# Kernel tuning notes

Measured on AMD Instinct MI355X. Metric: run time of the kernel, lower is better.

The kernel has to match this reference:

```python
import jax, jax.numpy as jnp
import numpy as np

EPS = 1e-7  # keras backend epsilon


def setup_inputs() -> dict:
    key = jax.random.key(0)
    k1, k2, k3, k4, k5 = jax.random.split(key, 5)
    B, L, D, U = 8, 1024, 256, 256
    seq_data = jax.random.normal(k1, (B, L, D), dtype=jnp.float32)
    graph = jax.random.uniform(k2, (B, L, L), dtype=jnp.float32)
    scale = 1.0 / np.sqrt(D)
    e_weight = jax.random.normal(k3, (D, U), dtype=jnp.float32) * scale
    Wx = jax.random.normal(k4, (U, U), dtype=jnp.float32) * scale
    Wh = jax.random.normal(k5, (U, U), dtype=jnp.float32) * scale
    b = jnp.zeros((U,), dtype=jnp.float32)
    return {"seq_data": seq_data, "graph": graph, "e_weight": e_weight,
            "Wx": Wx, "Wh": Wh, "b": b}


def reference(seq_data, graph, e_weight, Wx, Wh, b):
    # beta = seq_data @ e_weight : (B, L, U)
    beta = jnp.einsum('bld,du->blu', seq_data, e_weight)
    # normalize_graph_output: divide by out-degree sum over axis 2 -> (B, L)
    norm = jnp.maximum(jnp.sum(graph, axis=2), EPS)
    beta = beta / norm[:, :, None]
    # K.batch_dot(beta(B,L,U), graph(B,L,M), axes=(1,1)) -> (B,U,M), then
    # permute (0,2,1) -> (B,M,U); fused as a single einsum.
    agg = jnp.einsum('blu,blm->bmu', beta, graph)  # (B, L, U)
    B, L, U = agg.shape
    h0 = jnp.zeros((B, U), dtype=agg.dtype)  # get_initial_state: zeros

    def step(h, x):  # SimpleRNNCell: h' = tanh(x Wx + h Wh + b)
        h = jnp.tanh(x @ Wx + h @ Wh + b)
        return h, h

    _, ys = jax.lax.scan(step, h0, jnp.swapaxes(agg, 0, 1))  # (L, B, U)
    return jnp.swapaxes(ys, 0, 1)  # (B, L, U)
```

## Files before the change

### kernel.cpp

```cpp
#include <hip/hip_runtime.h>
#include <hip/hip_bf16.h>


typedef unsigned short u16;
typedef unsigned int u32;
typedef __bf16 bf16_t;
typedef __bf16 bf16x8 __attribute__((ext_vector_type(8)));
typedef float f32x4 __attribute__((ext_vector_type(4)));
typedef unsigned short u16x8 __attribute__((ext_vector_type(8)));
typedef unsigned short u16x4 __attribute__((ext_vector_type(4)));

#define LDS_P 72
#define HP_B  288

struct HiLo { u16 hi, lo; };

__device__ __forceinline__ u16 f2bf(float f) {
  bf16_t h = (bf16_t)f;
  return __builtin_bit_cast(u16, h);
}
__device__ __forceinline__ HiLo splitf(float v) {
  bf16_t h = (bf16_t)v;
  HiLo r;
  r.hi = __builtin_bit_cast(u16, h);
  r.lo = f2bf(v - (float)h);
  return r;
}
__device__ __forceinline__ float tanh_fast(float x) {
  float ax = fabsf(x);
  float e  = __expf(-2.0f * ax);
  float t  = __fdividef(1.0f - e, 1.0f + e);
  return copysignf(t, x);
}
__device__ __forceinline__ void sync_lds_only() {
  __asm__ volatile("s_waitcnt lgkmcnt(0)\ns_barrier" ::: "memory");
}

__global__ void transpose_split3(const float* __restrict__ s0, u16* __restrict__ h0, u16* __restrict__ l0,
                                 const float* __restrict__ s1, u16* __restrict__ h1, u16* __restrict__ l1,
                                 const float* __restrict__ s2, u16* __restrict__ h2o, u16* __restrict__ l2o) {
  const int u = blockIdx.x, d = threadIdx.x;
  const float* s; u16 *dh, *dl;
  if (blockIdx.y == 0)      { s = s0; dh = h0;  dl = l0; }
  else if (blockIdx.y == 1) { s = s1; dh = h1;  dl = l1; }
  else                      { s = s2; dh = h2o; dl = l2o; }
  HiLo r = splitf(s[d * 256 + u]);
  dh[u * 256 + d] = r.hi;
  dl[u * 256 + d] = r.lo;
}

__global__ void rowsum_norm(const float* __restrict__ graph, float* __restrict__ rnorm) {
  const int wave = threadIdx.x >> 6, lane = threadIdx.x & 63;
  const int row = blockIdx.x * 4 + wave;
  const float* p = graph + (size_t)row * 1024 + lane * 16;
  float s = 0.f;
#pragma unroll
  for (int c = 0; c < 4; c++) {
    f32x4 v = *(const f32x4*)(p + c * 4);
#pragma unroll
    for (int j = 0; j < 4; j++) s += v[j];
  }
#pragma unroll
  for (int off = 32; off > 0; off >>= 1) s += __shfl_xor(s, off);
  if (lane == 0) rnorm[row] = 1.0f / fmaxf(s, 1e-7f);
}

__global__ __launch_bounds__(256, 2) void gemm_beta(const float* __restrict__ seq,
                                                    const u16* __restrict__ Eth,
                                                    const u16* __restrict__ Etl,
                                                    const float* __restrict__ rnorm,
                                                    u16* __restrict__ betaTh,
                                                    u16* __restrict__ betaTl) {
  __shared__ u16 Ah[64 * LDS_P], Al[64 * LDS_P];
  __shared__ u16 Bh[64 * LDS_P], Bl[64 * LDS_P];
  const int t = threadIdx.x;
  const int wave = t >> 6, lane = t & 63, quad = lane >> 4, l16 = lane & 15;
  const int r0 = blockIdx.x * 64, n0 = blockIdx.y * 64;
  f32x4 acc[4];
#pragma unroll
  for (int i = 0; i < 4; i++) acc[i] = (f32x4){0.f, 0.f, 0.f, 0.f};

  for (int kb = 0; kb < 256; kb += 64) {
#pragma unroll
    for (int cc = 0; cc < 4; cc++) {
      int c = t + cc * 256;
      int r = c >> 4, c4 = c & 15;
      f32x4 v = *(const f32x4*)(seq + (size_t)(r0 + r) * 256 + kb + c4 * 4);
      u16x4 hi, lo;
#pragma unroll
      for (int j = 0; j < 4; j++) {
        HiLo s = splitf(v[j]);
        hi[j] = s.hi; lo[j] = s.lo;
      }
      *(u16x4*)(Ah + r * LDS_P + c4 * 4) = hi;
      *(u16x4*)(Al + r * LDS_P + c4 * 4) = lo;
    }
#pragma unroll
    for (int cc = 0; cc < 2; cc++) {
      int c = t + cc * 256;
      int r = c >> 3, c8 = c & 7;
      *(u16x8*)(Bh + r * LDS_P + c8 * 8) =
          *(const u16x8*)(Eth + (size_t)(n0 + r) * 256 + kb + c8 * 8);
      *(u16x8*)(Bl + r * LDS_P + c8 * 8) =
          *(const u16x8*)(Etl + (size_t)(n0 + r) * 256 + kb + c8 * 8);
    }
    __syncthreads();
#pragma unroll
    for (int kk = 0; kk < 64; kk += 32) {
      bf16x8 ah = __builtin_bit_cast(bf16x8, *(const u16x8*)(Ah + (wave * 16 + l16) * LDS_P + kk + quad * 8));
      bf16x8 al = __builtin_bit_cast(bf16x8, *(const u16x8*)(Al + (wave * 16 + l16) * LDS_P + kk + quad * 8));
#pragma unroll
      for (int tN = 0; tN < 4; tN++) {
        bf16x8 bh = __builtin_bit_cast(bf16x8, *(const u16x8*)(Bh + (tN * 16 + l16) * LDS_P + kk + quad * 8));
        bf16x8 bl = __builtin_bit_cast(bf16x8, *(const u16x8*)(Bl + (tN * 16 + l16) * LDS_P + kk + quad * 8));
        acc[tN] = __builtin_amdgcn_mfma_f32_16x16x32_bf16(ah, bh, acc[tN], 0, 0, 0);
        acc[tN] = __builtin_amdgcn_mfma_f32_16x16x32_bf16(ah, bl, acc[tN], 0, 0, 0);
        acc[tN] = __builtin_amdgcn_mfma_f32_16x16x32_bf16(al, bh, acc[tN], 0, 0, 0);
      }
    }
    __syncthreads();
  }
  const int rbase = r0 + wave * 16 + quad * 4;
  float rn[4];
#pragma unroll
  for (int i = 0; i < 4; i++) rn[i] = rnorm[rbase + i];
  const int bI = rbase >> 10, lI = rbase & 1023;
#pragma unroll
  for (int tN = 0; tN < 4; tN++) {
    int u = n0 + tN * 16 + l16;
    u16x4 hv, lv;
#pragma unroll
    for (int i = 0; i < 4; i++) {
      HiLo s = splitf(acc[tN][i] * rn[i]);
      hv[i] = s.hi; lv[i] = s.lo;
    }
    size_t off = ((size_t)bI << 18) + (size_t)u * 1024 + lI;
    *(u16x4*)(betaTh + off) = hv;
    *(u16x4*)(betaTl + off) = lv;
  }
}

__global__ __launch_bounds__(256, 2) void gemm_agg(const float* __restrict__ graph,
                                                   const u16* __restrict__ betaTh,
                                                   const u16* __restrict__ betaTl,
                                                   float* __restrict__ agg) {
  __shared__ u16 Ah[64 * LDS_P], Al[64 * LDS_P];
  __shared__ u16 Bh[64 * LDS_P], Bl[64 * LDS_P];
  const int t = threadIdx.x;
  const int wave = t >> 6, lane = t & 63, quad = lane >> 4, l16 = lane & 15;
  const int m0 = blockIdx.x * 64, n0 = blockIdx.y * 64, b = blockIdx.z;
  const float* g = graph + (size_t)b * (1024 * 1024);
  const size_t bt = (size_t)b << 18;
  f32x4 acc[4];
#pragma unroll
  for (int i = 0; i < 4; i++) acc[i] = (f32x4){0.f, 0.f, 0.f, 0.f};

  for (int kb = 0; kb < 1024; kb += 64) {
#pragma unroll
    for (int cc = 0; cc < 4; cc++) {
      int c = t + cc * 256;
      int r = c >> 4, c4 = c & 15;
      f32x4 v = *(const f32x4*)(g + (size_t)(kb + r) * 1024 + m0 + c4 * 4);
#pragma unroll
      for (int j = 0; j < 4; j++) {
        HiLo s = splitf(v[j]);
        Ah[(c4 * 4 + j) * LDS_P + r] = s.hi;
        Al[(c4 * 4 + j) * LDS_P + r] = s.lo;
      }
    }
#pragma unroll
    for (int cc = 0; cc < 2; cc++) {
      int c = t + cc * 256;
      int r = c >> 3, c8 = c & 7;
      *(u16x8*)(Bh + r * LDS_P + c8 * 8) =
          *(const u16x8*)(betaTh + bt + (size_t)(n0 + r) * 1024 + kb + c8 * 8);
      *(u16x8*)(Bl + r * LDS_P + c8 * 8) =
          *(const u16x8*)(betaTl + bt + (size_t)(n0 + r) * 1024 + kb + c8 * 8);
    }
    __syncthreads();
#pragma unroll
    for (int kk = 0; kk < 64; kk += 32) {
      bf16x8 ah = __builtin_bit_cast(bf16x8, *(const u16x8*)(Ah + (wave * 16 + l16) * LDS_P + kk + quad * 8));
      bf16x8 al = __builtin_bit_cast(bf16x8, *(const u16x8*)(Al + (wave * 16 + l16) * LDS_P + kk + quad * 8));
#pragma unroll
      for (int tN = 0; tN < 4; tN++) {
        bf16x8 bh = __builtin_bit_cast(bf16x8, *(const u16x8*)(Bh + (tN * 16 + l16) * LDS_P + kk + quad * 8));
        bf16x8 bl = __builtin_bit_cast(bf16x8, *(const u16x8*)(Bl + (tN * 16 + l16) * LDS_P + kk + quad * 8));
        acc[tN] = __builtin_amdgcn_mfma_f32_16x16x32_bf16(ah, bh, acc[tN], 0, 0, 0);
        acc[tN] = __builtin_amdgcn_mfma_f32_16x16x32_bf16(ah, bl, acc[tN], 0, 0, 0);
        acc[tN] = __builtin_amdgcn_mfma_f32_16x16x32_bf16(al, bh, acc[tN], 0, 0, 0);
      }
    }
    __syncthreads();
  }
  const int mbase = m0 + wave * 16 + quad * 4;
#pragma unroll
  for (int tN = 0; tN < 4; tN++) {
    int u = n0 + tN * 16 + l16;
#pragma unroll
    for (int i = 0; i < 4; i++)
      agg[((size_t)b * 1024 + mbase + i) * 256 + u] = acc[tN][i];
  }
}

__global__ __launch_bounds__(256, 2) void gemm_xpre(const float* __restrict__ agg,
                                                    const u16* __restrict__ Wxth,
                                                    const u16* __restrict__ Wxtl,
                                                    const float* __restrict__ bias,
                                                    float* __restrict__ Xpre) {
  __shared__ u16 Ah[64 * LDS_P], Al[64 * LDS_P];
  __shared__ u16 Bh[64 * LDS_P], Bl[64 * LDS_P];
  const int t = threadIdx.x;
  const int wave = t >> 6, lane = t & 63, quad = lane >> 4, l16 = lane & 15;
  const int r0 = blockIdx.x * 64, n0 = blockIdx.y * 64;
  f32x4 acc[4];
#pragma unroll
  for (int i = 0; i < 4; i++) acc[i] = (f32x4){0.f, 0.f, 0.f, 0.f};

  for (int kb = 0; kb < 256; kb += 64) {
#pragma unroll
    for (int cc = 0; cc < 4; cc++) {
      int c = t + cc * 256;
      int r = c >> 4, c4 = c & 15;
      f32x4 v = *(const f32x4*)(agg + (size_t)(r0 + r) * 256 + kb + c4 * 4);
      u16x4 hi, lo;
#pragma unroll
      for (int j = 0; j < 4; j++) {
        HiLo s = splitf(v[j]);
        hi[j] = s.hi; lo[j] = s.lo;
      }
      *(u16x4*)(Ah + r * LDS_P + c4 * 4) = hi;
      *(u16x4*)(Al + r * LDS_P + c4 * 4) = lo;
    }
#pragma unroll
    for (int cc = 0; cc < 2; cc++) {
      int c = t + cc * 256;
      int r = c >> 3, c8 = c & 7;
      *(u16x8*)(Bh + r * LDS_P + c8 * 8) =
          *(const u16x8*)(Wxth + (size_t)(n0 + r) * 256 + kb + c8 * 8);
      *(u16x8*)(Bl + r * LDS_P + c8 * 8) =
          *(const u16x8*)(Wxtl + (size_t)(n0 + r) * 256 + kb + c8 * 8);
    }
    __syncthreads();
#pragma unroll
    for (int kk = 0; kk < 64; kk += 32) {
      bf16x8 ah = __builtin_bit_cast(bf16x8, *(const u16x8*)(Ah + (wave * 16 + l16) * LDS_P + kk + quad * 8));
      bf16x8 al = __builtin_bit_cast(bf16x8, *(const u16x8*)(Al + (wave * 16 + l16) * LDS_P + kk + quad * 8));
#pragma unroll
      for (int tN = 0; tN < 4; tN++) {
        bf16x8 bh = __builtin_bit_cast(bf16x8, *(const u16x8*)(Bh + (tN * 16 + l16) * LDS_P + kk + quad * 8));
        bf16x8 bl = __builtin_bit_cast(bf16x8, *(const u16x8*)(Bl + (tN * 16 + l16) * LDS_P + kk + quad * 8));
        acc[tN] = __builtin_amdgcn_mfma_f32_16x16x32_bf16(ah, bh, acc[tN], 0, 0, 0);
        acc[tN] = __builtin_amdgcn_mfma_f32_16x16x32_bf16(ah, bl, acc[tN], 0, 0, 0);
        acc[tN] = __builtin_amdgcn_mfma_f32_16x16x32_bf16(al, bh, acc[tN], 0, 0, 0);
      }
    }
    __syncthreads();
  }
  const int rbase = r0 + wave * 16 + quad * 4;
  const int bI = rbase >> 10;
#pragma unroll
  for (int tN = 0; tN < 4; tN++) {
    int u = n0 + tN * 16 + l16;
    float bu = bias[u];
#pragma unroll
    for (int i = 0; i < 4; i++) {
      int mI = (rbase + i) & 1023;
      Xpre[((size_t)mI * 8 + bI) * 256 + u] = acc[tN][i] + bu;
    }
  }
}

__global__ __launch_bounds__(512, 2) void rnn_scan(const u16* __restrict__ Whth,
                                                   const u16* __restrict__ Whtl,
                                                   const float* __restrict__ Xpre,
                                                   float* __restrict__ out) {
  __shared__ u16 h2[2][2 * HP_B];
  const int b = blockIdx.x;
  const int t = threadIdx.x;
  const int w = t >> 6, lane = t & 63, quad = lane >> 4, l16 = lane & 15;
  const int colbase = w * 32;
  int col[2];
  col[0] = colbase + l16;
  col[1] = colbase + 16 + l16;
  const bool epi = (quad == 0);

  bf16x8 bwh[2][8], bwl[2][8];
#pragma unroll
  for (int tN = 0; tN < 2; tN++) {
    const u16* wph = Whth + (size_t)(colbase + tN * 16 + l16) * 256 + quad * 8;
    const u16* wpl = Whtl + (size_t)(colbase + tN * 16 + l16) * 256 + quad * 8;
#pragma unroll
    for (int kb = 0; kb < 8; kb++) {
      bwh[tN][kb] = __builtin_bit_cast(bf16x8, *(const u16x8*)(wph + kb * 32));
      bwl[tN][kb] = __builtin_bit_cast(bf16x8, *(const u16x8*)(wpl + kb * 32));
    }
  }
  for (int i = t; i < 2 * 2 * HP_B; i += 512) ((u16*)h2)[i] = 0;

  float cb[4][2];
#pragma unroll
  for (int k = 0; k < 4; k++) {
    const float* xp = Xpre + (size_t)k * 2048 + b * 256;
#pragma unroll
    for (int tt = 0; tt < 2; tt++) cb[k][tt] = xp[col[tt]];
  }
  const float* ldp = Xpre + 4 * 2048 + b * 256;
  float* outp = out + (size_t)b * 262144;
  const u16* rb0 = &h2[0][(l16 & 1) * HP_B + quad * 8];
  const u16* rb1 = &h2[1][(l16 & 1) * HP_B + quad * 8];
  u16* wb0 = &h2[0][0];
  u16* wb1 = &h2[1][0];
  __syncthreads();

  for (int m4 = 0; m4 < 1024; m4 += 4) {
#pragma unroll
    for (int k = 0; k < 4; k++) {
      const int p = k & 1;
      const u16* rb = p ? rb1 : rb0;
      u16* hw = p ? wb0 : wb1;

      f32x4 a0a = {0.f,0.f,0.f,0.f}, a0b = {0.f,0.f,0.f,0.f};
      f32x4 a1a = {0.f,0.f,0.f,0.f}, a1b = {0.f,0.f,0.f,0.f};
#pragma unroll
      for (int kb = 0; kb < 4; kb++) {
        bf16x8 afA = __builtin_bit_cast(bf16x8, *(const u16x8*)(rb + kb * 32));
        bf16x8 afB = __builtin_bit_cast(bf16x8, *(const u16x8*)(rb + (kb + 4) * 32));
        a0a = __builtin_amdgcn_mfma_f32_16x16x32_bf16(afA, bwh[0][kb], a0a, 0, 0, 0);
        a1a = __builtin_amdgcn_mfma_f32_16x16x32_bf16(afA, bwh[1][kb], a1a, 0, 0, 0);
        a0b = __builtin_amdgcn_mfma_f32_16x16x32_bf16(afB, bwh[0][kb + 4], a0b, 0, 0, 0);
        a1b = __builtin_amdgcn_mfma_f32_16x16x32_bf16(afB, bwh[1][kb + 4], a1b, 0, 0, 0);
        a0a = __builtin_amdgcn_mfma_f32_16x16x32_bf16(afA, bwl[0][kb], a0a, 0, 0, 0);
        a1a = __builtin_amdgcn_mfma_f32_16x16x32_bf16(afA, bwl[1][kb], a1a, 0, 0, 0);
        a0b = __builtin_amdgcn_mfma_f32_16x16x32_bf16(afB, bwl[0][kb + 4], a0b, 0, 0, 0);
        a1b = __builtin_amdgcn_mfma_f32_16x16x32_bf16(afB, bwl[1][kb + 4], a1b, 0, 0, 0);
      }

      if (epi) {
#pragma unroll
        for (int tt = 0; tt < 2; tt++) {
          float hi_part = (tt ? a1a[0] : a0a[0]) + (tt ? a1b[0] : a0b[0]);
          float lo_part = (tt ? a1a[1] : a0a[1]) + (tt ? a1b[1] : a0b[1]);
          float x = (hi_part + lo_part) + cb[k][tt];
          float y = tanh_fast(x);
          HiLo s = splitf(y);
          hw[col[tt]] = s.hi;
          hw[HP_B + col[tt]] = s.lo;
          outp[col[tt]] = y;
        }
      }
      outp += 256;

      if (m4 <= 1019 - k) {
#pragma unroll
        for (int tt = 0; tt < 2; tt++) cb[k][tt] = ldp[col[tt]];
        ldp += 2048;
      }
      sync_lds_only();
    }
  }
}

extern "C" void kernel_launch(void* const* d_in, const int* in_sizes, int n_in,
                              void* d_out, int out_size, void* d_ws, size_t ws_size,
                              hipStream_t stream) {
  (void)in_sizes; (void)n_in; (void)out_size; (void)ws_size;
  const float* seq   = (const float*)d_in[0];
  const float* graph = (const float*)d_in[1];
  const float* E     = (const float*)d_in[2];
  const float* Wx    = (const float*)d_in[3];
  const float* Wh    = (const float*)d_in[4];
  const float* bias  = (const float*)d_in[5];
  float* out = (float*)d_out;

  char* w = (char*)d_ws;
  float* rnorm  = (float*)(w + 0);
  u16*   Eth    = (u16*)(w + 32768);
  u16*   Etl    = (u16*)(w + 163840);
  u16*   Wxth   = (u16*)(w + 294912);
  u16*   Wxtl   = (u16*)(w + 425984);
  u16*   Whth   = (u16*)(w + 557056);
  u16*   Whtl   = (u16*)(w + 688128);
  u16*   betaTh = (u16*)(w + 819200);
  u16*   betaTl = (u16*)(w + 5013504);
  float* agg    = (float*)(w + 9207808);
  float* Xpre   = (float*)(w + 17596416);

  transpose_split3<<<dim3(256, 3), 256, 0, stream>>>(E, Eth, Etl, Wx, Wxth, Wxtl, Wh, Whth, Whtl);
  rowsum_norm<<<2048, 256, 0, stream>>>(graph, rnorm);
  gemm_beta<<<dim3(128, 4), 256, 0, stream>>>(seq, Eth, Etl, rnorm, betaTh, betaTl);
  gemm_agg<<<dim3(16, 4, 8), 256, 0, stream>>>(graph, betaTh, betaTl, agg);
  gemm_xpre<<<dim3(128, 4), 256, 0, stream>>>(agg, Wxth, Wxtl, bias, Xpre);
  rnn_scan<<<dim3(8), 512, 0, stream>>>(Whth, Whtl, Xpre, out);
}
```

Before: 837.7 us.

## Halve RNN scan block to 4 waves, each computing 64 columns

The sequential RNN scan kernel now uses 256 threads (4 waves) instead of 512, with each wave owning 64 output columns via four 16-wide MFMA tiles. Every lane now does epilogue work by selecting its quad's tile, where before only quad 0 did. The goal is to cut the per-step block barrier cost and idle lanes in the latency-bound recurrence. In exchange, each wave issues twice as many serial MFMAs per step and holds twice as many weight registers.

```diff
diff --git a/kernel.cpp b/kernel.cpp
--- a/kernel.cpp
+++ b/kernel.cpp
@@ -271,7 +271,7 @@
   }
 }
 
-__global__ __launch_bounds__(512, 2) void rnn_scan(const u16* __restrict__ Whth,
+__global__ __launch_bounds__(256, 1) void rnn_scan(const u16* __restrict__ Whth,
                                                    const u16* __restrict__ Whtl,
                                                    const float* __restrict__ Xpre,
                                                    float* __restrict__ out) {
@@ -279,15 +279,12 @@
   const int b = blockIdx.x;
   const int t = threadIdx.x;
   const int w = t >> 6, lane = t & 63, quad = lane >> 4, l16 = lane & 15;
-  const int colbase = w * 32;
-  int col[2];
-  col[0] = colbase + l16;
-  col[1] = colbase + 16 + l16;
-  const bool epi = (quad == 0);
-
-  bf16x8 bwh[2][8], bwl[2][8];
-#pragma unroll
-  for (int tN = 0; tN < 2; tN++) {
+  const int colbase = w * 64;
+  const int cwl = colbase + lane;
+
+  bf16x8 bwh[4][8], bwl[4][8];
+#pragma unroll
+  for (int tN = 0; tN < 4; tN++) {
     const u16* wph = Whth + (size_t)(colbase + tN * 16 + l16) * 256 + quad * 8;
     const u16* wpl = Whtl + (size_t)(colbase + tN * 16 + l16) * 256 + quad * 8;
 #pragma unroll
@@ -296,17 +293,13 @@
       bwl[tN][kb] = __builtin_bit_cast(bf16x8, *(const u16x8*)(wpl + kb * 32));
     }
   }
-  for (int i = t; i < 2 * 2 * HP_B; i += 512) ((u16*)h2)[i] = 0;
-
-  float cb[4][2];
-#pragma unroll
-  for (int k = 0; k < 4; k++) {
-    const float* xp = Xpre + (size_t)k * 2048 + b * 256;
-#pragma unroll
-    for (int tt = 0; tt < 2; tt++) cb[k][tt] = xp[col[tt]];
-  }
-  const float* ldp = Xpre + 4 * 2048 + b * 256;
-  float* outp = out + (size_t)b * 262144;
+  for (int i = t; i < 2 * 2 * HP_B; i += 256) ((u16*)h2)[i] = 0;
+
+  float cb[4];
+#pragma unroll
+  for (int k = 0; k < 4; k++) cb[k] = Xpre[(size_t)k * 2048 + b * 256 + cwl];
+  const float* ldp = Xpre + 4 * 2048 + b * 256 + cwl;
+  float* outp = out + (size_t)b * 262144 + cwl;
   const u16* rb0 = &h2[0][(l16 & 1) * HP_B + quad * 8];
   const u16* rb1 = &h2[1][(l16 & 1) * HP_B + quad * 8];
   u16* wb0 = &h2[0][0];
@@ -320,40 +313,43 @@
       const u16* rb = p ? rb1 : rb0;
       u16* hw = p ? wb0 : wb1;
 
-      f32x4 a0a = {0.f,0.f,0.f,0.f}, a0b = {0.f,0.f,0.f,0.f};
-      f32x4 a1a = {0.f,0.f,0.f,0.f}, a1b = {0.f,0.f,0.f,0.f};
+      f32x4 aA[4], aB[4];
+#pragma unroll
+      for (int i = 0; i < 4; i++) { aA[i] = (f32x4){0.f,0.f,0.f,0.f}; aB[i] = (f32x4){0.f,0.f,0.f,0.f}; }
 #pragma unroll
       for (int kb = 0; kb < 4; kb++) {
         bf16x8 afA = __builtin_bit_cast(bf16x8, *(const u16x8*)(rb + kb * 32));
         bf16x8 afB = __builtin_bit_cast(bf16x8, *(const u16x8*)(rb + (kb + 4) * 32));
-        a0a = __builtin_amdgcn_mfma_f32_16x16x32_bf16(afA, bwh[0][kb], a0a, 0, 0, 0);
-        a1a = __builtin_amdgcn_mfma_f32_16x16x32_bf16(afA, bwh[1][kb], a1a, 0, 0, 0);
-        a0b = __builtin_amdgcn_mfma_f32_16x16x32_bf16(afB, bwh[0][kb + 4], a0b, 0, 0, 0);
-        a1b = __builtin_amdgcn_mfma_f32_16x16x32_bf16(afB, bwh[1][kb + 4], a1b, 0, 0, 0);
-        a0a = __builtin_amdgcn_mfma_f32_16x16x32_bf16(afA, bwl[0][kb], a0a, 0, 0, 0);
-        a1a = __builtin_amdgcn_mfma_f32_16x16x32_bf16(afA, bwl[1][kb], a1a, 0, 0, 0);
-        a0b = __builtin_amdgcn_mfma_f32_16x16x32_bf16(afB, bwl[0][kb + 4], a0b, 0, 0, 0);
-        a1b = __builtin_amdgcn_mfma_f32_16x16x32_bf16(afB, bwl[1][kb + 4], a1b, 0, 0, 0);
-      }
-
-      if (epi) {
-#pragma unroll
-        for (int tt = 0; tt < 2; tt++) {
-          float hi_part = (tt ? a1a[0] : a0a[0]) + (tt ? a1b[0] : a0b[0]);
-          float lo_part = (tt ? a1a[1] : a0a[1]) + (tt ? a1b[1] : a0b[1]);
-          float x = (hi_part + lo_part) + cb[k][tt];
-          float y = tanh_fast(x);
-          HiLo s = splitf(y);
-          hw[col[tt]] = s.hi;
-          hw[HP_B + col[tt]] = s.lo;
-          outp[col[tt]] = y;
+#pragma unroll
+        for (int tN = 0; tN < 4; tN++) {
+          aA[tN] = __builtin_amdgcn_mfma_f32_16x16x32_bf16(afA, bwh[tN][kb], aA[tN], 0, 0, 0);
+          aB[tN] = __builtin_amdgcn_mfma_f32_16x16x32_bf16(afB, bwh[tN][kb + 4], aB[tN], 0, 0, 0);
         }
+#pragma unroll
+        for (int tN = 0; tN < 4; tN++) {
+          aA[tN] = __builtin_amdgcn_mfma_f32_16x16x32_bf16(afA, bwl[tN][kb], aA[tN], 0, 0, 0);
+          aB[tN] = __builtin_amdgcn_mfma_f32_16x16x32_bf16(afB, bwl[tN][kb + 4], aB[tN], 0, 0, 0);
+        }
+      }
+
+      {
+        float sA0 = quad < 2 ? (quad == 0 ? aA[0][0] : aA[1][0]) : (quad == 2 ? aA[2][0] : aA[3][0]);
+        float sA1 = quad < 2 ? (quad == 0 ? aA[0][1] : aA[1][1]) : (quad == 2 ? aA[2][1] : aA[3][1]);
+        float sB0 = quad < 2 ? (quad == 0 ? aB[0][0] : aB[1][0]) : (quad == 2 ? aB[2][0] : aB[3][0]);
+        float sB1 = quad < 2 ? (quad == 0 ? aB[0][1] : aB[1][1]) : (quad == 2 ? aB[2][1] : aB[3][1]);
+        float hi_part = sA0 + sB0;
+        float lo_part = sA1 + sB1;
+        float x = (hi_part + lo_part) + cb[k];
+        float y = tanh_fast(x);
+        HiLo s = splitf(y);
+        hw[cwl] = s.hi;
+        hw[HP_B + cwl] = s.lo;
+        *outp = y;
       }
       outp += 256;
 
       if (m4 <= 1019 - k) {
-#pragma unroll
-        for (int tt = 0; tt < 2; tt++) cb[k][tt] = ldp[col[tt]];
+        cb[k] = *ldp;
         ldp += 2048;
       }
       sync_lds_only();
@@ -391,5 +387,5 @@
   gemm_beta<<<dim3(128, 4), 256, 0, stream>>>(seq, Eth, Etl, rnorm, betaTh, betaTl);
   gemm_agg<<<dim3(16, 4, 8), 256, 0, stream>>>(graph, betaTh, betaTl, agg);
   gemm_xpre<<<dim3(128, 4), 256, 0, stream>>>(agg, Wxth, Wxtl, bias, Xpre);
-  rnn_scan<<<dim3(8), 512, 0, stream>>>(Whth, Whtl, Xpre, out);
-}
+  rnn_scan<<<dim3(8), 256, 0, stream>>>(Whth, Whtl, Xpre, out);
+}
```

Result: slower. 972.7 us (+16.1%).
